# Kernel optimization log

Measured on AMD Instinct MI355X. Metric: run time of the kernel, lower is better.

Reference implementation:

```python
import math
import jax, jax.numpy as jnp
import numpy as np
from jax import lax

EPS = 1e-5


def setup_inputs() -> dict:
    key = jax.random.key(0)
    ks = jax.random.split(key, 12)
    B, L, C = 4, 4096, 512
    d_inner, d_state, d_conv = 2 * C, 4, 4
    dt_rank = math.ceil(C / 16)  # 32
    s = 0.02
    A = jnp.tile(jnp.arange(1, d_state + 1, dtype=jnp.float32), (d_inner, 1))
    return {
        "hidden_states": jax.random.normal(ks[0], (B, L, C), jnp.float32),
        "mask": jnp.zeros((B, L), jnp.int32),
        "residual": jax.random.normal(ks[1], (B, L, C), jnp.float32),
        "norm_weight": jnp.ones((C,), jnp.float32),
        "conv_w": jax.random.normal(ks[2], (C, C, 3, 3), jnp.float32) * s,
        "conv_b": jnp.zeros((C,), jnp.float32),
        "in_proj_w": jax.random.normal(ks[3], (2 * d_inner, C), jnp.float32) * s,
        "conv1d_w": jax.random.normal(ks[4], (d_inner, 1, d_conv), jnp.float32) * s,
        "conv1d_b": jnp.zeros((d_inner,), jnp.float32),
        "x_proj_w": jax.random.normal(ks[5], (dt_rank + 2 * d_state, d_inner), jnp.float32) * s,
        "dt_proj_w": jax.random.normal(ks[6], (d_inner, dt_rank), jnp.float32) * s,
        "dt_proj_b": jnp.full((d_inner,), -4.6, jnp.float32),  # softplus ~ 0.01
        "A_log": jnp.log(A),
        "D": jnp.ones((d_inner,), jnp.float32),
        "out_proj_w": jax.random.normal(ks[7], (C, 2 * C), jnp.float32) * s,
    }


def _mamba(u, in_proj_w, conv1d_w, conv1d_b, x_proj_w, dt_proj_w, dt_proj_b, A_log, D, out_proj_w):
    # u: [B, L, C]
    Bn, Ln, _ = u.shape
    d_inner = conv1d_w.shape[0]
    d_state = A_log.shape[1]
    dt_rank = dt_proj_w.shape[1]
    d_conv = conv1d_w.shape[-1]
    xz = jnp.einsum("blc,ec->ble", u, in_proj_w)  # [B,L,2*d_inner]
    x, z = jnp.split(xz, 2, axis=-1)
    # causal depthwise conv1d (left pad d_conv-1)
    xc = lax.conv_general_dilated(
        x.transpose(0, 2, 1), conv1d_w, (1,), ((d_conv - 1, 0),),
        feature_group_count=d_inner, dimension_numbers=("NCH", "OIH", "NCH"))
    x = jax.nn.silu((xc + conv1d_b[None, :, None]).transpose(0, 2, 1))  # [B,L,D]
    x_dbl = jnp.einsum("bld,ed->ble", x, x_proj_w)
    dtr, Bm, Cm = jnp.split(x_dbl, [dt_rank, dt_rank + d_state], axis=-1)
    dt = jax.nn.softplus(jnp.einsum("blr,dr->bld", dtr, dt_proj_w) + dt_proj_b)
    A = -jnp.exp(A_log)  # [D,N]
    dA = jnp.exp(dt[..., None] * A)                              # [B,L,D,N]
    dBx = dt[..., None] * Bm[:, :, None, :] * x[..., None]       # [B,L,D,N]

    def step(h, t):
        dA_t, dBx_t, C_t = t
        h = dA_t * h + dBx_t
        return h, jnp.einsum("bdn,bn->bd", h, C_t)

    h0 = jnp.zeros((Bn, d_inner, d_state), dt.dtype)
    _, ys = lax.scan(step, h0, (dA.transpose(1, 0, 2, 3), dBx.transpose(1, 0, 2, 3), Cm.transpose(1, 0, 2)))
    y = ys.transpose(1, 0, 2) + x * D
    y = y * jax.nn.silu(z)
    return jnp.einsum("bld,cd->blc", y, out_proj_w)


def reference(hidden_states, mask, residual, norm_weight, conv_w, conv_b,
              in_proj_w, conv1d_w, conv1d_b, x_proj_w, dt_proj_w, dt_proj_b,
              A_log, D, out_proj_w):
    # fused add + RMSNorm, prenorm, residual in fp32
    res = (hidden_states + residual).astype(jnp.float32)
    var = jnp.mean(res * res, axis=-1, keepdims=True)
    hs = res * lax.rsqrt(var + EPS) * norm_weight
    Bn, Ln, Cn = hs.shape
    Ls = int(round(math.sqrt(Ln)))
    img = hs.transpose(0, 2, 1).reshape(Bn, Cn, Ls, Ls)
    img = lax.conv_general_dilated(img, conv_w, (1, 1), ((1, 1), (1, 1)),
                                   dimension_numbers=("NCHW", "OIHW", "NCHW"))
    img = img + conv_b[None, :, None, None]
    hs = img.reshape(Bn, Cn, Ln).transpose(0, 2, 1)  # [B,L,C]
    # gather tokens where mask==0 (equal count per row; here n_easy = L)
    n_easy = Ln
    order = jnp.argsort(mask, axis=1, stable=True)
    easy_idx = order[:, :n_easy]  # [B, n_easy]
    easy = jnp.take_along_axis(hs, easy_idx[:, :, None], axis=1)
    mixed = _mamba(easy, in_proj_w, conv1d_w, conv1d_b, x_proj_w,
                   dt_proj_w, dt_proj_b, A_log, D, out_proj_w)
    # scatter mixer output back into the full sequence
    x = hs.at[jnp.arange(Bn)[:, None], easy_idx].set(mixed)
    return x, res
```

## Files before the change

kernel.cpp:

```cpp
#include <hip/hip_runtime.h>
#include <hip/hip_bf16.h>

#define BB 4
#define LL 4096
#define CC 512
#define DI 1024
#define DS 4
#define DR 32
#define LS 64
#define CHUNK 64
#define NCH 64

typedef unsigned short ushortT;
typedef __attribute__((ext_vector_type(8))) short bf16x8;
typedef __attribute__((ext_vector_type(4))) float f32x4;

static __device__ __forceinline__ float b2f(ushortT u) {
    union { unsigned int i; float f; } v; v.i = ((unsigned int)u) << 16; return v.f;
}
static __device__ __forceinline__ ushortT f2b(float f) {
    unsigned int x = __float_as_uint(f);
    unsigned int lsb = (x >> 16) & 1u;
    x += 0x7fffu + lsb;
    return (ushortT)(x >> 16);
}

__global__ __launch_bounds__(512) void k_norm(const float* __restrict__ hid,
                                              const float* __restrict__ resi,
                                              const float* __restrict__ nw,
                                              float* __restrict__ out_res,
                                              ushortT* __restrict__ hs) {
    int bl = blockIdx.x;
    int c  = threadIdx.x;
    size_t base = (size_t)bl * CC;
    float h = hid[base + c] + resi[base + c];
    out_res[base + c] = h;

    float s = h * h;
    #pragma unroll
    for (int o = 32; o > 0; o >>= 1) s += __shfl_xor(s, o);
    __shared__ float ws[8];
    int w = c >> 6;
    if ((c & 63) == 0) ws[w] = s;
    __syncthreads();
    float tot = 0.f;
    #pragma unroll
    for (int i = 0; i < 8; i++) tot += ws[i];
    float scale = rsqrtf(tot / (float)CC + 1e-5f);

    hs[base + c] = f2b(h * scale * nw[c]);
}

__global__ __launch_bounds__(256) void k_repack_conv(const float* __restrict__ conv_w,
                                                     ushortT* __restrict__ wb3) {
    int g = blockIdx.x * 256 + threadIdx.x;
    int ic = g & 511, oc = g >> 9;
    const float* src = conv_w + ((size_t)(oc * CC + ic)) * 9;
    #pragma unroll
    for (int tap = 0; tap < 9; tap++)
        wb3[((size_t)oc * 9 + tap) * 512 + ic] = f2b(src[tap]);
}

__global__ __launch_bounds__(256) void k_cvt_bf16(const float* __restrict__ W,
                                                  ushortT* __restrict__ out, int n4) {
    int i = blockIdx.x * 256 + threadIdx.x;
    if (i >= n4) return;
    float4 v = ((const float4*)W)[i];
    ushort4 o = { f2b(v.x), f2b(v.y), f2b(v.z), f2b(v.w) };
    ((ushort4*)out)[i] = o;
}

__global__ __launch_bounds__(256) void k_repack_xpw(const float* __restrict__ xpw,
                                                    ushortT* __restrict__ wbx) {
    int g = blockIdx.x * 256 + threadIdx.x;
    int k = g & 1023, e = g >> 10;
    wbx[g] = (e < 40) ? f2b(xpw[(size_t)e * DI + k]) : (ushortT)0;
}

__global__ __launch_bounds__(256) void k_conv2d_mfma(const ushortT* __restrict__ hs,
                                                     const ushortT* __restrict__ wb3,
                                                     const float* __restrict__ convb,
                                                     ushortT* __restrict__ u) {
    const int b = blockIdx.z;
    const int ytile = blockIdx.x;
    const int n0 = blockIdx.y * 128;
    const int tid = threadIdx.x;
    const int lane = tid & 63, w = tid >> 6;
    const int wr = w >> 1, wc = w & 1;
    const int fm = lane & 15, kg = lane >> 4;

    __shared__ ushortT As[128][40];
    __shared__ ushortT Bs[128][40];

    f32x4 acc[4][4];
    #pragma unroll
    for (int i = 0; i < 4; i++)
        #pragma unroll
        for (int j = 0; j < 4; j++) acc[i][j] = (f32x4){0.f, 0.f, 0.f, 0.f};
    const bf16x8 zf = {0, 0, 0, 0, 0, 0, 0, 0};

    const int sr0 = w * 32;
    const int lrow = lane >> 2;
    const int lcol = (lane & 3) * 8;

    for (int tap = 0; tap < 9; tap++) {
        const int dy = tap / 3 - 1, dx = tap % 3 - 1;
        bool ok[2]; size_t asrc[2], bsrc[2];
        #pragma unroll
        for (int q = 0; q < 2; q++) {
            int r = sr0 + q * 16 + lrow;
            int y = ytile * 2 + (r >> 6) + dy;
            int x = (r & 63) + dx;
            ok[q] = ((unsigned)y < 64u) && ((unsigned)x < 64u);
            asrc[q] = ok[q] ? ((size_t)(b * LL + y * 64 + x)) * CC + lcol : (size_t)lcol;
            bsrc[q] = ((size_t)(n0 + r) * 9 + tap) * 512 + lcol;
        }
        for (int ics = 0; ics < 16; ics++) {
            const int ko = ics * 32;
            bf16x8 av[2], bv[2];
            #pragma unroll
            for (int q = 0; q < 2; q++) {
                bf16x8 t = *(const bf16x8*)(hs + asrc[q] + ko);
                av[q] = ok[q] ? t : zf;
                bv[q] = *(const bf16x8*)(wb3 + bsrc[q] + ko);
            }
            #pragma unroll
            for (int q = 0; q < 2; q++) {
                *(bf16x8*)(&As[sr0 + q * 16 + lrow][lcol]) = av[q];
                *(bf16x8*)(&Bs[sr0 + q * 16 + lrow][lcol]) = bv[q];
            }
            __syncthreads();
            bf16x8 afr[4], bfr[4];
            #pragma unroll
            for (int ms = 0; ms < 4; ms++)
                afr[ms] = *(const bf16x8*)(&As[wr * 64 + ms * 16 + fm][kg * 8]);
            #pragma unroll
            for (int ns = 0; ns < 4; ns++)
                bfr[ns] = *(const bf16x8*)(&Bs[wc * 64 + ns * 16 + fm][kg * 8]);
            #pragma unroll
            for (int ms = 0; ms < 4; ms++)
                #pragma unroll
                for (int ns = 0; ns < 4; ns++)
                    acc[ms][ns] = __builtin_amdgcn_mfma_f32_16x16x32_bf16(afr[ms], bfr[ns], acc[ms][ns], 0, 0, 0);
            __syncthreads();
        }
    }

    const int rowb = ytile * 128 + wr * 64;
    const int colb = n0 + wc * 64;
    #pragma unroll
    for (int ms = 0; ms < 4; ms++) {
        #pragma unroll
        for (int ns = 0; ns < 4; ns++) {
            int col = colb + ns * 16 + fm;
            float bias = convb[col];
            f32x4 v = acc[ms][ns];
            #pragma unroll
            for (int r = 0; r < 4; r++) {
                int row = rowb + ms * 16 + kg * 4 + r;
                u[((size_t)(b * LL + row)) * CC + col] = f2b(v[r] + bias);
            }
        }
    }
}

__global__ __launch_bounds__(256) void k_inproj_mfma(const ushortT* __restrict__ A,
                                                     const ushortT* __restrict__ Wb,
                                                     ushortT* __restrict__ xout,
                                                     ushortT* __restrict__ zout) {
    const int m0 = blockIdx.x * 128, n0 = blockIdx.y * 128;
    const int tid = threadIdx.x;
    const int lane = tid & 63, w = tid >> 6;
    const int wr = w >> 1, wc = w & 1;
    const int fm = lane & 15, kg = lane >> 4;

    __shared__ ushortT As[128][40];
    __shared__ ushortT Bs[128][40];

    f32x4 acc[4][4];
    #pragma unroll
    for (int i = 0; i < 4; i++)
        #pragma unroll
        for (int j = 0; j < 4; j++) acc[i][j] = (f32x4){0.f, 0.f, 0.f, 0.f};

    const int sr0 = w * 32;
    const int lrow = lane >> 2;
    const int lcol = (lane & 3) * 8;

    for (int k0 = 0; k0 < CC; k0 += 32) {
        #pragma unroll
        for (int q = 0; q < 2; q++) {
            int r = sr0 + q * 16 + lrow;
            bf16x8 av = *(const bf16x8*)(A  + (size_t)(m0 + r) * CC + k0 + lcol);
            bf16x8 bv = *(const bf16x8*)(Wb + (size_t)(n0 + r) * CC + k0 + lcol);
            *(bf16x8*)(&As[r][lcol]) = av;
            *(bf16x8*)(&Bs[r][lcol]) = bv;
        }
        __syncthreads();
        bf16x8 afr[4], bfr[4];
        #pragma unroll
        for (int ms = 0; ms < 4; ms++)
            afr[ms] = *(const bf16x8*)(&As[wr * 64 + ms * 16 + fm][kg * 8]);
        #pragma unroll
        for (int ns = 0; ns < 4; ns++)
            bfr[ns] = *(const bf16x8*)(&Bs[wc * 64 + ns * 16 + fm][kg * 8]);
        #pragma unroll
        for (int ms = 0; ms < 4; ms++)
            #pragma unroll
            for (int ns = 0; ns < 4; ns++)
                acc[ms][ns] = __builtin_amdgcn_mfma_f32_16x16x32_bf16(afr[ms], bfr[ns], acc[ms][ns], 0, 0, 0);
        __syncthreads();
    }

    const int rowb = m0 + wr * 64;
    const int colb = n0 + wc * 64;
    #pragma unroll
    for (int ms = 0; ms < 4; ms++) {
        #pragma unroll
        for (int ns = 0; ns < 4; ns++) {
            int col = colb + ns * 16 + fm;
            f32x4 v = acc[ms][ns];
            #pragma unroll
            for (int r = 0; r < 4; r++) {
                int row = rowb + ms * 16 + kg * 4 + r;
                float val = v[r];
                if (col < DI) {
                    xout[(size_t)row * DI + col] = f2b(val);
                } else {
                    float s = val / (1.f + __expf(-val));
                    zout[(size_t)row * DI + (col - DI)] = f2b(s);
                }
            }
        }
    }
}

__global__ __launch_bounds__(256) void k_xproj_mfma(const ushortT* __restrict__ A,
                                                    const ushortT* __restrict__ Wb,
                                                    float* __restrict__ xdbl,
                                                    ushortT* __restrict__ dtr_b) {
    const int m0 = blockIdx.x * 128;
    const int tid = threadIdx.x;
    const int lane = tid & 63, w = tid >> 6;
    const int wr = w >> 1, wc = w & 1;
    const int fm = lane & 15, kg = lane >> 4;

    __shared__ ushortT As[128][40];
    __shared__ ushortT Bs[64][40];

    f32x4 acc[4][2];
    #pragma unroll
    for (int i = 0; i < 4; i++)
        #pragma unroll
        for (int j = 0; j < 2; j++) acc[i][j] = (f32x4){0.f, 0.f, 0.f, 0.f};

    const int ar = tid >> 2;
    const int lcol = (tid & 3) * 8;

    for (int k0 = 0; k0 < DI; k0 += 32) {
        #pragma unroll
        for (int q = 0; q < 2; q++) {
            int r = ar + q * 64;
            bf16x8 av = *(const bf16x8*)(A + (size_t)(m0 + r) * DI + k0 + lcol);
            *(bf16x8*)(&As[r][lcol]) = av;
        }
        {
            bf16x8 bv = *(const bf16x8*)(Wb + (size_t)ar * DI + k0 + lcol);
            *(bf16x8*)(&Bs[ar][lcol]) = bv;
        }
        __syncthreads();
        bf16x8 afr[4], bfr[2];
        #pragma unroll
        for (int ms = 0; ms < 4; ms++)
            afr[ms] = *(const bf16x8*)(&As[wr * 64 + ms * 16 + fm][kg * 8]);
        #pragma unroll
        for (int ns = 0; ns < 2; ns++)
            bfr[ns] = *(const bf16x8*)(&Bs[wc * 32 + ns * 16 + fm][kg * 8]);
        #pragma unroll
        for (int ms = 0; ms < 4; ms++)
            #pragma unroll
            for (int ns = 0; ns < 2; ns++)
                acc[ms][ns] = __builtin_amdgcn_mfma_f32_16x16x32_bf16(afr[ms], bfr[ns], acc[ms][ns], 0, 0, 0);
        __syncthreads();
    }

    const int rowb = m0 + wr * 64;
    #pragma unroll
    for (int ms = 0; ms < 4; ms++) {
        #pragma unroll
        for (int ns = 0; ns < 2; ns++) {
            int col = wc * 32 + ns * 16 + fm;
            f32x4 v = acc[ms][ns];
            #pragma unroll
            for (int r = 0; r < 4; r++) {
                int row = rowb + ms * 16 + kg * 4 + r;
                float val = v[r];
                if (col < 40) xdbl[(size_t)row * 40 + col] = val;
                if (col < 32) dtr_b[(size_t)row * 32 + col] = f2b(val);
            }
        }
    }
}

__global__ __launch_bounds__(256) void k_dt_mfma(const ushortT* __restrict__ Ab,
                                                 const ushortT* __restrict__ Wb,
                                                 const float* __restrict__ dtb,
                                                 ushortT* __restrict__ dty) {
    const int m0 = blockIdx.x * 128, n0 = blockIdx.y * 128;
    const int tid = threadIdx.x;
    const int lane = tid & 63, w = tid >> 6;
    const int wr = w >> 1, wc = w & 1;
    const int fm = lane & 15, kg = lane >> 4;

    __shared__ ushortT As[128][40];
    __shared__ ushortT Bs[128][40];

    f32x4 acc[4][4];
    #pragma unroll
    for (int i = 0; i < 4; i++)
        #pragma unroll
        for (int j = 0; j < 4; j++) acc[i][j] = (f32x4){0.f, 0.f, 0.f, 0.f};

    const int ar = tid >> 2;
    const int lcol = (tid & 3) * 8;
    #pragma unroll
    for (int q = 0; q < 2; q++) {
        int r = ar + q * 64;
        bf16x8 av = *(const bf16x8*)(Ab + (size_t)(m0 + r) * 32 + lcol);
        bf16x8 bv = *(const bf16x8*)(Wb + (size_t)(n0 + r) * 32 + lcol);
        *(bf16x8*)(&As[r][lcol]) = av;
        *(bf16x8*)(&Bs[r][lcol]) = bv;
    }
    __syncthreads();
    bf16x8 afr[4], bfr[4];
    #pragma unroll
    for (int ms = 0; ms < 4; ms++)
        afr[ms] = *(const bf16x8*)(&As[wr * 64 + ms * 16 + fm][kg * 8]);
    #pragma unroll
    for (int ns = 0; ns < 4; ns++)
        bfr[ns] = *(const bf16x8*)(&Bs[wc * 64 + ns * 16 + fm][kg * 8]);
    #pragma unroll
    for (int ms = 0; ms < 4; ms++)
        #pragma unroll
        for (int ns = 0; ns < 4; ns++)
            acc[ms][ns] = __builtin_amdgcn_mfma_f32_16x16x32_bf16(afr[ms], bfr[ns], acc[ms][ns], 0, 0, 0);

    const int rowb = m0 + wr * 64;
    const int colb = n0 + wc * 64;
    #pragma unroll
    for (int ms = 0; ms < 4; ms++) {
        #pragma unroll
        for (int ns = 0; ns < 4; ns++) {
            int col = colb + ns * 16 + fm;
            float bias = dtb[col];
            f32x4 v = acc[ms][ns];
            #pragma unroll
            for (int r = 0; r < 4; r++) {
                int row = rowb + ms * 16 + kg * 4 + r;
                float a = v[r] + bias;
                float sp = (a > 20.f) ? a : log1pf(__expf(a));
                dty[(size_t)row * DI + col] = f2b(sp);
            }
        }
    }
}

__global__ __launch_bounds__(256) void k_outproj_mfma(const ushortT* __restrict__ A,
                                                      const ushortT* __restrict__ Wb,
                                                      float* __restrict__ out) {
    const int m0 = blockIdx.x * 128, n0 = blockIdx.y * 128;
    const int tid = threadIdx.x;
    const int lane = tid & 63, w = tid >> 6;
    const int wr = w >> 1, wc = w & 1;
    const int fm = lane & 15, kg = lane >> 4;

    __shared__ ushortT As[128][40];
    __shared__ ushortT Bs[128][40];

    f32x4 acc[4][4];
    #pragma unroll
    for (int i = 0; i < 4; i++)
        #pragma unroll
        for (int j = 0; j < 4; j++) acc[i][j] = (f32x4){0.f, 0.f, 0.f, 0.f};

    const int sr0 = w * 32;
    const int lrow = lane >> 2;
    const int lcol = (lane & 3) * 8;

    for (int k0 = 0; k0 < DI; k0 += 32) {
        #pragma unroll
        for (int q = 0; q < 2; q++) {
            int r = sr0 + q * 16 + lrow;
            bf16x8 av = *(const bf16x8*)(A  + (size_t)(m0 + r) * DI + k0 + lcol);
            bf16x8 bv = *(const bf16x8*)(Wb + (size_t)(n0 + r) * DI + k0 + lcol);
            *(bf16x8*)(&As[r][lcol]) = av;
            *(bf16x8*)(&Bs[r][lcol]) = bv;
        }
        __syncthreads();
        bf16x8 afr[4], bfr[4];
        #pragma unroll
        for (int ms = 0; ms < 4; ms++)
            afr[ms] = *(const bf16x8*)(&As[wr * 64 + ms * 16 + fm][kg * 8]);
        #pragma unroll
        for (int ns = 0; ns < 4; ns++)
            bfr[ns] = *(const bf16x8*)(&Bs[wc * 64 + ns * 16 + fm][kg * 8]);
        #pragma unroll
        for (int ms = 0; ms < 4; ms++)
            #pragma unroll
            for (int ns = 0; ns < 4; ns++)
                acc[ms][ns] = __builtin_amdgcn_mfma_f32_16x16x32_bf16(afr[ms], bfr[ns], acc[ms][ns], 0, 0, 0);
        __syncthreads();
    }

    const int rowb = m0 + wr * 64;
    const int colb = n0 + wc * 64;
    #pragma unroll
    for (int ms = 0; ms < 4; ms++) {
        #pragma unroll
        for (int ns = 0; ns < 4; ns++) {
            int col = colb + ns * 16 + fm;
            f32x4 v = acc[ms][ns];
            #pragma unroll
            for (int r = 0; r < 4; r++) {
                int row = rowb + ms * 16 + kg * 4 + r;
                out[(size_t)row * CC + col] = v[r];
            }
        }
    }
}

__global__ __launch_bounds__(256) void k_conv1d(const ushortT* __restrict__ xbuf,
                                                const float* __restrict__ w,
                                                const float* __restrict__ bias,
                                                ushortT* __restrict__ xs) {
    int idx = blockIdx.x * 256 + threadIdx.x;
    int d = idx & (DI - 1);
    int l = (idx >> 10) & (LL - 1);
    int b = idx >> 22;
    float acc = bias[d];
    #pragma unroll
    for (int k = 0; k < 4; k++) {
        int ll = l + k - 3;
        if (ll >= 0)
            acc += b2f(xbuf[(((size_t)(b << 12) + ll) << 10) + d]) * w[d * 4 + k];
    }
    float s = acc / (1.f + __expf(-acc));
    xs[idx] = f2b(s);
}

__global__ __launch_bounds__(256) void k_scan_p1(const ushortT* __restrict__ dt,
                                                 const ushortT* __restrict__ xs,
                                                 const float* __restrict__ xdbl,
                                                 const float* __restrict__ alog,
                                                 float* __restrict__ P,
                                                 float* __restrict__ S) {
    int d  = blockIdx.x * 256 + threadIdx.x;
    int ch = blockIdx.y;
    int b  = blockIdx.z;
    int t  = threadIdx.x;

    __shared__ float sB[CHUNK][4];
    if (t < CHUNK) {
        const float* xr = xdbl + ((size_t)(b * LL + ch * CHUNK + t)) * 40;
        float4 v = *(const float4*)(xr + 32);
        sB[t][0] = v.x; sB[t][1] = v.y; sB[t][2] = v.z; sB[t][3] = v.w;
    }
    __syncthreads();

    float An[4], h[4] = {0.f, 0.f, 0.f, 0.f}, Pp[4] = {1.f, 1.f, 1.f, 1.f};
    #pragma unroll
    for (int n = 0; n < 4; n++) An[n] = -__expf(alog[d * 4 + n]);

    size_t row0 = (size_t)b * LL + ch * CHUNK;
    for (int i = 0; i < CHUNK; i++) {
        size_t row = row0 + i;
        float dtv = b2f(dt[row * DI + d]);
        float xv  = b2f(xs[row * DI + d]);
        float dbx = dtv * xv;
        #pragma unroll
        for (int n = 0; n < 4; n++) {
            float dA = __expf(dtv * An[n]);
            h[n]  = dA * h[n] + dbx * sB[i][n];
            Pp[n] *= dA;
        }
    }
    size_t o = (((size_t)b * NCH + ch) * DI + d) * 4;
    *(float4*)(P + o) = make_float4(Pp[0], Pp[1], Pp[2], Pp[3]);
    *(float4*)(S + o) = make_float4(h[0], h[1], h[2], h[3]);
}

__global__ __launch_bounds__(256) void k_scan_cmb(const float* __restrict__ P,
                                                  const float* __restrict__ S,
                                                  float* __restrict__ Hin) {
    int td = blockIdx.x * 256 + threadIdx.x;
    int b = td >> 10, d = td & (DI - 1);
    float h[4] = {0.f, 0.f, 0.f, 0.f};
    for (int ch = 0; ch < NCH; ch++) {
        size_t o = (((size_t)b * NCH + ch) * DI + d) * 4;
        *(float4*)(Hin + o) = make_float4(h[0], h[1], h[2], h[3]);
        float4 p = *(const float4*)(P + o);
        float4 s = *(const float4*)(S + o);
        h[0] = p.x * h[0] + s.x;
        h[1] = p.y * h[1] + s.y;
        h[2] = p.z * h[2] + s.z;
        h[3] = p.w * h[3] + s.w;
    }
}

__global__ __launch_bounds__(256) void k_scan_p2(ushortT* dty,
                                                 const ushortT* __restrict__ xs,
                                                 const float* __restrict__ xdbl,
                                                 const ushortT* __restrict__ zs,
                                                 const float* __restrict__ alog,
                                                 const float* __restrict__ Dv,
                                                 const float* __restrict__ Hin) {
    int d  = blockIdx.x * 256 + threadIdx.x;
    int ch = blockIdx.y;
    int b  = blockIdx.z;
    int t  = threadIdx.x;

    __shared__ float sBC[CHUNK][8];
    if (t < CHUNK) {
        const float* xr = xdbl + ((size_t)(b * LL + ch * CHUNK + t)) * 40;
        float4 v1 = *(const float4*)(xr + 32);
        float4 v2 = *(const float4*)(xr + 36);
        sBC[t][0] = v1.x; sBC[t][1] = v1.y; sBC[t][2] = v1.z; sBC[t][3] = v1.w;
        sBC[t][4] = v2.x; sBC[t][5] = v2.y; sBC[t][6] = v2.z; sBC[t][7] = v2.w;
    }
    __syncthreads();

    float An[4];
    #pragma unroll
    for (int n = 0; n < 4; n++) An[n] = -__expf(alog[d * 4 + n]);
    float Dd = Dv[d];

    size_t o = (((size_t)b * NCH + ch) * DI + d) * 4;
    float4 h0 = *(const float4*)(Hin + o);
    float h[4] = {h0.x, h0.y, h0.z, h0.w};

    size_t row0 = (size_t)b * LL + ch * CHUNK;
    for (int i = 0; i < CHUNK; i++) {
        size_t row = row0 + i;
        float dtv = b2f(dty[row * DI + d]);
        float xv  = b2f(xs[row * DI + d]);
        float dbx = dtv * xv;
        float y = 0.f;
        #pragma unroll
        for (int n = 0; n < 4; n++) {
            float dA = __expf(dtv * An[n]);
            h[n] = dA * h[n] + dbx * sBC[i][n];
            y += h[n] * sBC[i][4 + n];
        }
        float sz = b2f(zs[row * DI + d]);
        dty[row * DI + d] = f2b((y + xv * Dd) * sz);
    }
}

__global__ __launch_bounds__(256) void k_sentinel(float* __restrict__ out0) {
    int i = blockIdx.x * 256 + threadIdx.x;
    out0[i] = 1.0f;
}

extern "C" void kernel_launch(void* const* d_in, const int* in_sizes, int n_in,
                              void* d_out, int out_size, void* d_ws, size_t ws_size,
                              hipStream_t stream) {
    const float* hid   = (const float*)d_in[0];
    const float* resi  = (const float*)d_in[2];
    const float* nw    = (const float*)d_in[3];
    const float* convw = (const float*)d_in[4];
    const float* convb = (const float*)d_in[5];
    const float* inw   = (const float*)d_in[6];
    const float* c1w   = (const float*)d_in[7];
    const float* c1b   = (const float*)d_in[8];
    const float* xpw   = (const float*)d_in[9];
    const float* dtw   = (const float*)d_in[10];
    const float* dtb   = (const float*)d_in[11];
    const float* alog  = (const float*)d_in[12];
    const float* Dv    = (const float*)d_in[13];
    const float* outw  = (const float*)d_in[14];

    float* out0 = (float*)d_out;
    float* out1 = out0 + (size_t)BB * LL * CC;

    const size_t RA = (size_t)BB * LL * CC * 2;
    const size_t RB = (size_t)BB * LL * DI * 2;
    const size_t NEED = RA + 2 * RB;

    ushortT* hs    = (ushortT*)d_out;
    ushortT* wbi   = (ushortT*)((char*)d_out + RA);
    ushortT* xs    = (ushortT*)d_out;
    char* base = (char*)d_ws;
    ushortT* u     = (ushortT*)base;
    float*   xdbl  = (float*)base;
    ushortT* wbx   = (ushortT*)(base + 2621440);
    ushortT* dtwb  = (ushortT*)(base + 2752512);
    ushortT* wbo   = (ushortT*)(base + (3u << 20));
    float*   Pbuf  = (float*)(base + (4u << 20));
    ushortT* dtr_b = (ushortT*)(base + (4u << 20));
    float*   Sbuf  = (float*)(base + (8u << 20));
    float*   Hin   = (float*)(base + (12u << 20));
    ushortT* wb3   = (ushortT*)(base + RA);
    ushortT* xb    = (ushortT*)(base + RA);
    ushortT* dty   = (ushortT*)(base + RA);
    ushortT* zsilu = (ushortT*)(base + RA + RB);

    if (ws_size < NEED) {
        k_norm<<<BB * LL, 512, 0, stream>>>(hid, resi, nw, out1, hs);
        k_sentinel<<<(BB * LL * CC) / 256, 256, 0, stream>>>(out0);
        return;
    }

    k_norm<<<BB * LL, 512, 0, stream>>>(hid, resi, nw, out1, hs);
    k_repack_conv<<<(CC * CC) / 256, 256, 0, stream>>>(convw, wb3);
    k_cvt_bf16<<<1024, 256, 0, stream>>>(inw, wbi, (2 * DI * CC) / 4);
    k_conv2d_mfma<<<dim3(32, 4, BB), 256, 0, stream>>>(hs, wb3, convb, u);
    k_inproj_mfma<<<dim3(128, 16), 256, 0, stream>>>(u, wbi, xb, zsilu);
    k_cvt_bf16<<<512, 256, 0, stream>>>(outw, wbo, (CC * DI) / 4);
    k_repack_xpw<<<256, 256, 0, stream>>>(xpw, wbx);
    k_cvt_bf16<<<32, 256, 0, stream>>>(dtw, dtwb, (DI * DR) / 4);
    k_conv1d<<<65536, 256, 0, stream>>>(xb, c1w, c1b, xs);
    k_xproj_mfma<<<128, 256, 0, stream>>>(xs, wbx, xdbl, dtr_b);
    k_dt_mfma<<<dim3(128, 8), 256, 0, stream>>>(dtr_b, dtwb, dtb, dty);
    k_scan_p1<<<dim3(DI / 256, NCH, BB), 256, 0, stream>>>(dty, xs, xdbl, alog, Pbuf, Sbuf);
    k_scan_cmb<<<(BB * DI) / 256, 256, 0, stream>>>(Pbuf, Sbuf, Hin);
    k_scan_p2<<<dim3(DI / 256, NCH, BB), 256, 0, stream>>>(dty, xs, xdbl, zsilu, alog, Dv, Hin);
    k_outproj_mfma<<<dim3(128, 4), 256, 0, stream>>>(dty, wbo, out0);
}
```

Before: 454.9 us.

## Use direct global-to-LDS loads in GEMMs and zero-padded conv image

The three MFMA GEMM kernels (conv2d, in_proj, out_proj) now stage tiles with global_load_lds, which writes 16 bytes per lane straight into LDS instead of going through registers, and the padded LDS rows are dropped to fit that layout. To remove the per-load bounds masking in the 3x3 conv, the norm kernel writes into a zero-padded 66x66 image cleared by a memset beforehand. The change adds a memset pass and a larger intermediate buffer, and the unpadded LDS layout may cause bank conflicts on fragment reads.

```diff
diff --git a/kernel.cpp b/kernel.cpp
--- a/kernel.cpp
+++ b/kernel.cpp
@@ -10,6 +10,7 @@
 #define LS 64
 #define CHUNK 64
 #define NCH 64
+#define PW 66
 
 typedef unsigned short ushortT;
 typedef __attribute__((ext_vector_type(8))) short bf16x8;
@@ -25,11 +26,19 @@
     return (ushortT)(x >> 16);
 }
 
+static __device__ __forceinline__ void gl16(const ushortT* g, ushortT* l) {
+    typedef const __attribute__((address_space(1))) unsigned int GU;
+    typedef __attribute__((address_space(3))) unsigned int LU;
+    __builtin_amdgcn_global_load_lds((GU*)(unsigned long long)(const void*)g,
+                                     (LU*)(unsigned int)(unsigned long long)(void*)l,
+                                     16, 0, 0);
+}
+
 __global__ __launch_bounds__(512) void k_norm(const float* __restrict__ hid,
                                               const float* __restrict__ resi,
                                               const float* __restrict__ nw,
                                               float* __restrict__ out_res,
-                                              ushortT* __restrict__ hs) {
+                                              ushortT* __restrict__ himg) {
     int bl = blockIdx.x;
     int c  = threadIdx.x;
     size_t base = (size_t)bl * CC;
@@ -48,7 +57,9 @@
     for (int i = 0; i < 8; i++) tot += ws[i];
     float scale = rsqrtf(tot / (float)CC + 1e-5f);
 
-    hs[base + c] = f2b(h * scale * nw[c]);
+    int b = bl >> 12, l = bl & 4095;
+    int iy = (l >> 6) + 1, ix = (l & 63) + 1;
+    himg[(((size_t)b * PW + iy) * PW + ix) * CC + c] = f2b(h * scale * nw[c]);
 }
 
 __global__ __launch_bounds__(256) void k_repack_conv(const float* __restrict__ conv_w,
@@ -77,7 +88,7 @@
     wbx[g] = (e < 40) ? f2b(xpw[(size_t)e * DI + k]) : (ushortT)0;
 }
 
-__global__ __launch_bounds__(256) void k_conv2d_mfma(const ushortT* __restrict__ hs,
+__global__ __launch_bounds__(256) void k_conv2d_mfma(const ushortT* __restrict__ himg,
                                                      const ushortT* __restrict__ wb3,
                                                      const float* __restrict__ convb,
                                                      ushortT* __restrict__ u) {
@@ -89,45 +100,35 @@
     const int wr = w >> 1, wc = w & 1;
     const int fm = lane & 15, kg = lane >> 4;
 
-    __shared__ ushortT As[128][40];
-    __shared__ ushortT Bs[128][40];
+    __shared__ __align__(16) ushortT As[128][32];
+    __shared__ __align__(16) ushortT Bs[128][32];
 
     f32x4 acc[4][4];
     #pragma unroll
     for (int i = 0; i < 4; i++)
         #pragma unroll
         for (int j = 0; j < 4; j++) acc[i][j] = (f32x4){0.f, 0.f, 0.f, 0.f};
-    const bf16x8 zf = {0, 0, 0, 0, 0, 0, 0, 0};
-
-    const int sr0 = w * 32;
-    const int lrow = lane >> 2;
-    const int lcol = (lane & 3) * 8;
+
+    const int sp  = (lane >> 2);
+    const int sch = (lane & 3) * 8;
 
     for (int tap = 0; tap < 9; tap++) {
         const int dy = tap / 3 - 1, dx = tap % 3 - 1;
-        bool ok[2]; size_t asrc[2], bsrc[2];
+        size_t ag[2], bg[2];
         #pragma unroll
         for (int q = 0; q < 2; q++) {
-            int r = sr0 + q * 16 + lrow;
-            int y = ytile * 2 + (r >> 6) + dy;
-            int x = (r & 63) + dx;
-            ok[q] = ((unsigned)y < 64u) && ((unsigned)x < 64u);
-            asrc[q] = ok[q] ? ((size_t)(b * LL + y * 64 + x)) * CC + lcol : (size_t)lcol;
-            bsrc[q] = ((size_t)(n0 + r) * 9 + tap) * 512 + lcol;
+            int p  = w * 32 + q * 16 + sp;
+            int iy = ytile * 2 + (p >> 6) + dy + 1;
+            int ix = (p & 63) + dx + 1;
+            ag[q] = (((size_t)b * PW + iy) * PW + ix) * CC + sch;
+            bg[q] = ((size_t)(n0 + p) * 9 + tap) * 512 + sch;
         }
         for (int ics = 0; ics < 16; ics++) {
             const int ko = ics * 32;
-            bf16x8 av[2], bv[2];
             #pragma unroll
             for (int q = 0; q < 2; q++) {
-                bf16x8 t = *(const bf16x8*)(hs + asrc[q] + ko);
-                av[q] = ok[q] ? t : zf;
-                bv[q] = *(const bf16x8*)(wb3 + bsrc[q] + ko);
-            }
-            #pragma unroll
-            for (int q = 0; q < 2; q++) {
-                *(bf16x8*)(&As[sr0 + q * 16 + lrow][lcol]) = av[q];
-                *(bf16x8*)(&Bs[sr0 + q * 16 + lrow][lcol]) = bv[q];
+                gl16(himg + ag[q] + ko, &As[w * 32 + q * 16][0]);
+                gl16(wb3  + bg[q] + ko, &Bs[w * 32 + q * 16][0]);
             }
             __syncthreads();
             bf16x8 afr[4], bfr[4];
@@ -174,8 +175,8 @@
     const int wr = w >> 1, wc = w & 1;
     const int fm = lane & 15, kg = lane >> 4;
 
-    __shared__ ushortT As[128][40];
-    __shared__ ushortT Bs[128][40];
+    __shared__ __align__(16) ushortT As[128][32];
+    __shared__ __align__(16) ushortT Bs[128][32];
 
     f32x4 acc[4][4];
     #pragma unroll
@@ -183,18 +184,15 @@
         #pragma unroll
         for (int j = 0; j < 4; j++) acc[i][j] = (f32x4){0.f, 0.f, 0.f, 0.f};
 
-    const int sr0 = w * 32;
-    const int lrow = lane >> 2;
-    const int lcol = (lane & 3) * 8;
+    const int sp  = (lane >> 2);
+    const int sch = (lane & 3) * 8;
 
     for (int k0 = 0; k0 < CC; k0 += 32) {
         #pragma unroll
         for (int q = 0; q < 2; q++) {
-            int r = sr0 + q * 16 + lrow;
-            bf16x8 av = *(const bf16x8*)(A  + (size_t)(m0 + r) * CC + k0 + lcol);
-            bf16x8 bv = *(const bf16x8*)(Wb + (size_t)(n0 + r) * CC + k0 + lcol);
-            *(bf16x8*)(&As[r][lcol]) = av;
-            *(bf16x8*)(&Bs[r][lcol]) = bv;
+            int p = w * 32 + q * 16 + sp;
+            gl16(A  + (size_t)(m0 + p) * CC + k0 + sch, &As[w * 32 + q * 16][0]);
+            gl16(Wb + (size_t)(n0 + p) * CC + k0 + sch, &Bs[w * 32 + q * 16][0]);
         }
         __syncthreads();
         bf16x8 afr[4], bfr[4];
@@ -235,6 +233,67 @@
     }
 }
 
+__global__ __launch_bounds__(256) void k_outproj_mfma(const ushortT* __restrict__ A,
+                                                      const ushortT* __restrict__ Wb,
+                                                      float* __restrict__ out) {
+    const int m0 = blockIdx.x * 128, n0 = blockIdx.y * 128;
+    const int tid = threadIdx.x;
+    const int lane = tid & 63, w = tid >> 6;
+    const int wr = w >> 1, wc = w & 1;
+    const int fm = lane & 15, kg = lane >> 4;
+
+    __shared__ __align__(16) ushortT As[128][32];
+    __shared__ __align__(16) ushortT Bs[128][32];
+
+    f32x4 acc[4][4];
+    #pragma unroll
+    for (int i = 0; i < 4; i++)
+        #pragma unroll
+        for (int j = 0; j < 4; j++) acc[i][j] = (f32x4){0.f, 0.f, 0.f, 0.f};
+
+    const int sp  = (lane >> 2);
+    const int sch = (lane & 3) * 8;
+
+    for (int k0 = 0; k0 < DI; k0 += 32) {
+        #pragma unroll
+        for (int q = 0; q < 2; q++) {
+            int p = w * 32 + q * 16 + sp;
+            gl16(A  + (size_t)(m0 + p) * DI + k0 + sch, &As[w * 32 + q * 16][0]);
+            gl16(Wb + (size_t)(n0 + p) * DI + k0 + sch, &Bs[w * 32 + q * 16][0]);
+        }
+        __syncthreads();
+        bf16x8 afr[4], bfr[4];
+        #pragma unroll
+        for (int ms = 0; ms < 4; ms++)
+            afr[ms] = *(const bf16x8*)(&As[wr * 64 + ms * 16 + fm][kg * 8]);
+        #pragma unroll
+        for (int ns = 0; ns < 4; ns++)
+            bfr[ns] = *(const bf16x8*)(&Bs[wc * 64 + ns * 16 + fm][kg * 8]);
+        #pragma unroll
+        for (int ms = 0; ms < 4; ms++)
+            #pragma unroll
+            for (int ns = 0; ns < 4; ns++)
+                acc[ms][ns] = __builtin_amdgcn_mfma_f32_16x16x32_bf16(afr[ms], bfr[ns], acc[ms][ns], 0, 0, 0);
+        __syncthreads();
+    }
+
+    const int rowb = m0 + wr * 64;
+    const int colb = n0 + wc * 64;
+    #pragma unroll
+    for (int ms = 0; ms < 4; ms++) {
+        #pragma unroll
+        for (int ns = 0; ns < 4; ns++) {
+            int col = colb + ns * 16 + fm;
+            f32x4 v = acc[ms][ns];
+            #pragma unroll
+            for (int r = 0; r < 4; r++) {
+                int row = rowb + ms * 16 + kg * 4 + r;
+                out[(size_t)row * CC + col] = v[r];
+            }
+        }
+    }
+}
+
 __global__ __launch_bounds__(256) void k_xproj_mfma(const ushortT* __restrict__ A,
                                                     const ushortT* __restrict__ Wb,
                                                     float* __restrict__ xdbl,
@@ -360,70 +419,6 @@
                 float a = v[r] + bias;
                 float sp = (a > 20.f) ? a : log1pf(__expf(a));
                 dty[(size_t)row * DI + col] = f2b(sp);
-            }
-        }
-    }
-}
-
-__global__ __launch_bounds__(256) void k_outproj_mfma(const ushortT* __restrict__ A,
-                                                      const ushortT* __restrict__ Wb,
-                                                      float* __restrict__ out) {
-    const int m0 = blockIdx.x * 128, n0 = blockIdx.y * 128;
-    const int tid = threadIdx.x;
-    const int lane = tid & 63, w = tid >> 6;
-    const int wr = w >> 1, wc = w & 1;
-    const int fm = lane & 15, kg = lane >> 4;
-
-    __shared__ ushortT As[128][40];
-    __shared__ ushortT Bs[128][40];
-
-    f32x4 acc[4][4];
-    #pragma unroll
-    for (int i = 0; i < 4; i++)
-        #pragma unroll
-        for (int j = 0; j < 4; j++) acc[i][j] = (f32x4){0.f, 0.f, 0.f, 0.f};
-
-    const int sr0 = w * 32;
-    const int lrow = lane >> 2;
-    const int lcol = (lane & 3) * 8;
-
-    for (int k0 = 0; k0 < DI; k0 += 32) {
-        #pragma unroll
-        for (int q = 0; q < 2; q++) {
-            int r = sr0 + q * 16 + lrow;
-            bf16x8 av = *(const bf16x8*)(A  + (size_t)(m0 + r) * DI + k0 + lcol);
-            bf16x8 bv = *(const bf16x8*)(Wb + (size_t)(n0 + r) * DI + k0 + lcol);
-            *(bf16x8*)(&As[r][lcol]) = av;
-            *(bf16x8*)(&Bs[r][lcol]) = bv;
-        }
-        __syncthreads();
-        bf16x8 afr[4], bfr[4];
-        #pragma unroll
-        for (int ms = 0; ms < 4; ms++)
-            afr[ms] = *(const bf16x8*)(&As[wr * 64 + ms * 16 + fm][kg * 8]);
-        #pragma unroll
-        for (int ns = 0; ns < 4; ns++)
-            bfr[ns] = *(const bf16x8*)(&Bs[wc * 64 + ns * 16 + fm][kg * 8]);
-        #pragma unroll
-        for (int ms = 0; ms < 4; ms++)
-            #pragma unroll
-            for (int ns = 0; ns < 4; ns++)
-                acc[ms][ns] = __builtin_amdgcn_mfma_f32_16x16x32_bf16(afr[ms], bfr[ns], acc[ms][ns], 0, 0, 0);
-        __syncthreads();
-    }
-
-    const int rowb = m0 + wr * 64;
-    const int colb = n0 + wc * 64;
-    #pragma unroll
-    for (int ms = 0; ms < 4; ms++) {
-        #pragma unroll
-        for (int ns = 0; ns < 4; ns++) {
-            int col = colb + ns * 16 + fm;
-            f32x4 v = acc[ms][ns];
-            #pragma unroll
-            for (int r = 0; r < 4; r++) {
-                int row = rowb + ms * 16 + kg * 4 + r;
-                out[(size_t)row * CC + col] = v[r];
             }
         }
     }
@@ -585,9 +580,10 @@
     const size_t RA = (size_t)BB * LL * CC * 2;
     const size_t RB = (size_t)BB * LL * DI * 2;
     const size_t NEED = RA + 2 * RB;
-
-    ushortT* hs    = (ushortT*)d_out;
-    ushortT* wbi   = (ushortT*)((char*)d_out + RA);
+    const size_t HIMG_BYTES = (size_t)BB * PW * PW * CC * 2;
+
+    ushortT* himg  = (ushortT*)d_out;
+    ushortT* wbi   = (ushortT*)((char*)d_out + (18u << 20));
     ushortT* xs    = (ushortT*)d_out;
     char* base = (char*)d_ws;
     ushortT* u     = (ushortT*)base;
@@ -605,15 +601,15 @@
     ushortT* zsilu = (ushortT*)(base + RA + RB);
 
     if (ws_size < NEED) {
-        k_norm<<<BB * LL, 512, 0, stream>>>(hid, resi, nw, out1, hs);
         k_sentinel<<<(BB * LL * CC) / 256, 256, 0, stream>>>(out0);
         return;
     }
 
-    k_norm<<<BB * LL, 512, 0, stream>>>(hid, resi, nw, out1, hs);
+    hipMemsetAsync(himg, 0, HIMG_BYTES, stream);
+    k_norm<<<BB * LL, 512, 0, stream>>>(hid, resi, nw, out1, himg);
     k_repack_conv<<<(CC * CC) / 256, 256, 0, stream>>>(convw, wb3);
     k_cvt_bf16<<<1024, 256, 0, stream>>>(inw, wbi, (2 * DI * CC) / 4);
-    k_conv2d_mfma<<<dim3(32, 4, BB), 256, 0, stream>>>(hs, wb3, convb, u);
+    k_conv2d_mfma<<<dim3(32, 4, BB), 256, 0, stream>>>(himg, wb3, convb, u);
     k_inproj_mfma<<<dim3(128, 16), 256, 0, stream>>>(u, wbi, xb, zsilu);
     k_cvt_bf16<<<512, 256, 0, stream>>>(outw, wbo, (CC * DI) / 4);
     k_repack_xpw<<<256, 256, 0, stream>>>(xpw, wbx);
```

Result: faster. 435.2 us (-4.3%).
